# Performance work log

Measured on AMD Instinct MI355X. Metric: run time of the kernel, lower is better.

## Reference

```python
import jax, jax.numpy as jnp
import numpy as np

B, L, D, H = 64, 256, 512, 512


def setup_inputs() -> dict:
    key = jax.random.key(0)
    ks = jax.random.split(key, 17)
    s = 1.0 / np.sqrt(D + H)  # torch nn.Linear default init bound

    def w(k):
        return jax.random.uniform(k, (H, D + H), minval=-s, maxval=s, dtype=jnp.float32)

    def b(k):
        return jax.random.uniform(k, (H,), minval=-s, maxval=s, dtype=jnp.float32)

    inp = {"x": jax.random.normal(ks[0], (B, L, D), dtype=jnp.float32)}
    names = ["f", "i", "o", "g"]
    idx = 1
    for d in ("fw", "bw"):
        for n in names:
            kw, kb = jax.random.split(ks[idx])
            inp[f"W_{d}_{n}"] = w(kw)
            inp[f"b_{d}_{n}"] = b(kb)
            idx += 1
    return inp


def _make_cell(Wf, bf, Wi, bi, Wo, bo, Wg, bg):
    def cell(carry, xt):
        h, c = carry
        comb = jnp.concatenate([xt, h], axis=1)  # (B, D+H)
        ft = jax.nn.sigmoid(comb @ Wf.T + bf)
        it = jax.nn.sigmoid(comb @ Wi.T + bi)
        ot = jax.nn.sigmoid(comb @ Wo.T + bo)
        gt = jnp.tanh(comb @ Wg.T + bg)
        c = ft * c + it * gt
        h = ot * jnp.tanh(c)
        return (h, c), h
    return cell


def reference(x, W_fw_f, b_fw_f, W_fw_i, b_fw_i, W_fw_o, b_fw_o, W_fw_g, b_fw_g,
              W_bw_f, b_bw_f, W_bw_i, b_bw_i, W_bw_o, b_bw_o, W_bw_g, b_bw_g):
    Bx, Lx, _ = x.shape
    Hx = W_fw_f.shape[0]
    h0 = jnp.zeros((Bx, Hx), x.dtype)
    c0 = jnp.zeros((Bx, Hx), x.dtype)
    xs = jnp.swapaxes(x, 0, 1)  # (L, B, D) time-major

    _, hf = jax.lax.scan(_make_cell(W_fw_f, b_fw_f, W_fw_i, b_fw_i, W_fw_o, b_fw_o, W_fw_g, b_fw_g), (h0, c0), xs)
    _, hb = jax.lax.scan(_make_cell(W_bw_f, b_bw_f, W_bw_i, b_bw_i, W_bw_o, b_bw_o, W_bw_g, b_bw_g), (h0, c0), xs[::-1])
    hb = hb[::-1]  # hidden_b.reverse() in original

    # Faithful to original: stack time-major, flatten, hstack, reshape(B, L, 2H)
    flat = jnp.concatenate([hf.reshape(-1, Hx), hb.reshape(-1, Hx)], axis=1)  # (L*B, 2H)
    return flat.reshape(Bx, Lx, 2 * Hx)
```

## Files before the change

### kernel.cpp

```cpp
#include <hip/hip_runtime.h>

typedef unsigned short u16;
typedef unsigned int u32;
typedef unsigned long long u64;
typedef __bf16 bf16x8 __attribute__((ext_vector_type(8)));
typedef float f32x4 __attribute__((ext_vector_type(4)));

#define OFF_XPROJ 0ull
#define OFF_XBF   134217728ull
#define OFF_WXBF  150994944ull
#define OFF_BIAS  155189248ull
#define OFF_HRING 134217728ull
#define NSLOT 160
#define RESET_D 8

struct WPtrs { const float* p[8]; };

__device__ __forceinline__ u16 f2bf(float f) {
    __bf16 h = (__bf16)f;
    return __builtin_bit_cast(u16, h);
}
__device__ __forceinline__ float bf2f(u16 u) {
    __bf16 h = __builtin_bit_cast(__bf16, u);
    return (float)h;
}
__device__ __forceinline__ u32 pack2(float a, float b) {
    return (u32)f2bf(a) | ((u32)f2bf(b) << 16);
}
__device__ __forceinline__ float sigf(float x) {
    return __builtin_amdgcn_rcpf(1.0f + __expf(-x));
}
__device__ __forceinline__ float tanhfast(float x) {
    float a = fabsf(x);
    float e = __expf(-2.0f * a);
    float t = (1.0f - e) * __builtin_amdgcn_rcpf(1.0f + e);
    return copysignf(t, x);
}
__device__ __forceinline__ bool is_canary(u64 v) {
    return ((u32)v == 0xFFFFFFFFu) | ((u32)(v >> 32) == 0xFFFFFFFFu);
}

__global__ void __launch_bounds__(256) pack_x(const float* __restrict__ x, u16* __restrict__ xbf) {
    int idx = blockIdx.x * 256 + threadIdx.x;
    int e = idx * 4;
    float4 v = *(const float4*)(x + e);
    xbf[e+0] = f2bf(v.x); xbf[e+1] = f2bf(v.y);
    xbf[e+2] = f2bf(v.z); xbf[e+3] = f2bf(v.w);
}

__global__ void __launch_bounds__(256) pack_w(WPtrs wp, u16* __restrict__ wxbf) {
    int idx = blockIdx.x * 256 + threadIdx.x;
    int e = idx * 4;
    int n = e >> 9;
    int k = e & 511;
    int j = n & 511, g = (n >> 9) & 3, d = n >> 11;
    const float* W = wp.p[d*4 + g];
    float4 v = *(const float4*)(W + j*1024 + k);
    wxbf[n*512 + k + 0] = f2bf(v.x); wxbf[n*512 + k + 1] = f2bf(v.y);
    wxbf[n*512 + k + 2] = f2bf(v.z); wxbf[n*512 + k + 3] = f2bf(v.w);
}

__global__ void __launch_bounds__(256) pack_bias(WPtrs bp, u16* __restrict__ biasws) {
    int idx = blockIdx.x * 256 + threadIdx.x;
    int j = idx & 511, g = (idx >> 9) & 3, d = idx >> 11;
    biasws[idx] = f2bf(bp.p[d*4 + g][j]);
}

__global__ void __launch_bounds__(256) init_hring(u16* __restrict__ ring) {
    size_t idx = (size_t)blockIdx.x * 256 + threadIdx.x;
    size_t byte = idx * 16;
    size_t seg = byte % 10485760ull;
    uint4 v;
    if (seg < 65536ull) { v.x = 0u; v.y = 0u; v.z = 0u; v.w = 0u; }
    else                { v.x = ~0u; v.y = ~0u; v.z = ~0u; v.w = ~0u; }
    *(uint4*)((char*)ring + byte) = v;
}

__global__ void __launch_bounds__(256) gemm_xproj(const u16* __restrict__ xbf,
                                                  const u16* __restrict__ wxbf,
                                                  const u16* __restrict__ biasws,
                                                  u16* __restrict__ xproj) {
    __shared__ u16 A[64 * 264];
    int tid = threadIdx.x, w = tid >> 6, lane = tid & 63, q = lane >> 4, ln = lane & 15;
    int mb = blockIdx.x >> 6, nb = blockIdx.x & 63;
    int n = nb*64 + w*16 + ln;

    bf16x8 bfr[16];
    #pragma unroll
    for (int kk = 0; kk < 16; ++kk)
        bfr[kk] = *(const bf16x8*)(wxbf + n*512 + kk*32 + q*8);
    float bias = bf2f(biasws[n]);

    f32x4 acc[4] = {{0.f,0.f,0.f,0.f},{0.f,0.f,0.f,0.f},{0.f,0.f,0.f,0.f},{0.f,0.f,0.f,0.f}};
    const u16* Abase = xbf + (size_t)mb * 64 * 512;

    for (int half = 0; half < 2; ++half) {
        for (int it = 0; it < 8; ++it) {
            int idx = tid + it*256;
            int r = idx >> 5, c = idx & 31;
            *(uint4*)&A[r*264 + c*8] = *(const uint4*)(Abase + r*512 + half*256 + c*8);
        }
        __syncthreads();
        #pragma unroll
        for (int kk = 0; kk < 8; ++kk) {
            #pragma unroll
            for (int mt = 0; mt < 4; ++mt) {
                bf16x8 af = *(const bf16x8*)&A[(mt*16 + ln)*264 + kk*32 + q*8];
                acc[mt] = __builtin_amdgcn_mfma_f32_16x16x32_bf16(af, bfr[half*8 + kk], acc[mt], 0, 0, 0);
            }
        }
        __syncthreads();
    }

    int dd = n >> 11, gg = (n >> 9) & 3, jj = n & 511;
    #pragma unroll
    for (int mt = 0; mt < 4; ++mt) {
        #pragma unroll
        for (int r2 = 0; r2 < 4; ++r2) {
            int m = mb*64 + mt*16 + q*4 + r2;
            int t = m & 255, b = m >> 8;
            float v = acc[mt][r2] + bias;
            xproj[(size_t)((dd*256 + t)*64 + b) * 2048 + gg*512 + jj] = f2bf(v);
        }
    }
}

__global__ void __launch_bounds__(256) bilstm_rec(const u16* __restrict__ xproj,
                                                  u16* __restrict__ hring,
                                                  float* __restrict__ out,
                                                  WPtrs wp) {
    __shared__ u16 A[64 * 256];
    __shared__ float pre[4 * 64 * 17];

    int tid = threadIdx.x, w = tid >> 6, lane = tid & 63, q = lane >> 4, ln = lane & 15;
    int d = blockIdx.x >> 5, cb = blockIdx.x & 31, j0 = cb * 16;
    int b = tid >> 2, hc0 = (tid & 3) * 4;
    int col8h = tid & 63, rb = tid >> 7;
    bool phB = (tid & 64) != 0;

    const float* Wg = wp.p[d*4 + w];
    bf16x8 bfr[16];
    #pragma unroll
    for (int kk = 0; kk < 16; ++kk) {
        const float* src = Wg + (j0 + ln)*1024 + 512 + kk*32 + q*8;
        float4 v0 = *(const float4*)src;
        float4 v1 = *(const float4*)(src + 4);
        bf16x8 t;
        t[0]=(__bf16)v0.x; t[1]=(__bf16)v0.y; t[2]=(__bf16)v0.z; t[3]=(__bf16)v0.w;
        t[4]=(__bf16)v1.x; t[5]=(__bf16)v1.y; t[6]=(__bf16)v1.z; t[7]=(__bf16)v1.w;
        bfr[kk] = t;
    }

    float cre[4] = {0.f, 0.f, 0.f, 0.f};

    u64 xp4[4];
    {
        int t0 = d ? 255 : 0;
        const u16* xp_t = xproj + ((size_t)((d*256 + t0)*64 + b))*2048 + j0 + hc0;
        #pragma unroll
        for (int g = 0; g < 4; ++g) xp4[g] = *(const u64*)(xp_t + g*512);
    }

    for (int s = 0; s < 256; ++s) {
        int t_ = d ? (255 - s) : s;
        int sl = s;      if (sl >= NSLOT) sl -= NSLOT;
        int sw = s + 1;  if (sw >= NSLOT) sw -= NSLOT;
        int sr = s + 1 + RESET_D; if (sr >= NSLOT) sr -= NSLOT;
        const u64* hsrc = (const u64*)hring + ((size_t)(d*NSLOT + sl)) * 8192;

        u64 vv[32];
        {
            u64 v0 = __hip_atomic_load(hsrc + tid, __ATOMIC_RELAXED, __HIP_MEMORY_SCOPE_AGENT);
            while (is_canary(v0)) {
                __builtin_amdgcn_s_sleep(1);
                v0 = __hip_atomic_load(hsrc + tid, __ATOMIC_RELAXED, __HIP_MEMORY_SCOPE_AGENT);
            }
            vv[0] = v0;
        }
        #pragma unroll
        for (int it = 1; it < 32; ++it)
            vv[it] = __hip_atomic_load(hsrc + it*256 + tid, __ATOMIC_RELAXED, __HIP_MEMORY_SCOPE_AGENT);
        u32 pend = 0;
        #pragma unroll
        for (int it = 1; it < 32; ++it)
            if (is_canary(vv[it])) pend |= (1u << it);
        while (__builtin_expect(pend != 0u, 0)) {
            __builtin_amdgcn_s_sleep(1);
            u32 np = 0;
            #pragma unroll
            for (int it = 1; it < 32; ++it)
                if (pend & (1u << it)) {
                    u64 v = __hip_atomic_load(hsrc + it*256 + tid, __ATOMIC_RELAXED, __HIP_MEMORY_SCOPE_AGENT);
                    if (is_canary(v)) np |= (1u << it);
                    else vv[it] = v;
                }
            pend = np;
        }

        f32x4 acc[4] = {{0.f,0.f,0.f,0.f},{0.f,0.f,0.f,0.f},{0.f,0.f,0.f,0.f},{0.f,0.f,0.f,0.f}};

        if (!phB) {
            #pragma unroll
            for (int it = 0; it < 32; ++it) {
                int row = it*2 + rb;
                int off = row*512 + ((((col8h >> 1) ^ (row & 7)) << 4) | ((col8h & 1) << 3));
                *(u64*)((char*)A + off) = vv[it];
            }
        }
        __syncthreads();
        #pragma unroll
        for (int kk = 0; kk < 8; ++kk) {
            #pragma unroll
            for (int mt = 0; mt < 4; ++mt) {
                int row = mt*16 + ln;
                bf16x8 af = *(const bf16x8*)((const char*)A + row*512 + (((kk*4 + q) ^ (ln & 7)) << 4));
                acc[mt] = __builtin_amdgcn_mfma_f32_16x16x32_bf16(af, bfr[kk], acc[mt], 0, 0, 0);
            }
        }
        __syncthreads();

        if (phB) {
            #pragma unroll
            for (int it = 0; it < 32; ++it) {
                int row = it*2 + rb;
                int off = row*512 + ((((col8h >> 1) ^ (row & 7)) << 4) | ((col8h & 1) << 3));
                *(u64*)((char*)A + off) = vv[it];
            }
        }
        __syncthreads();
        #pragma unroll
        for (int kk = 0; kk < 8; ++kk) {
            #pragma unroll
            for (int mt = 0; mt < 4; ++mt) {
                int row = mt*16 + ln;
                bf16x8 af = *(const bf16x8*)((const char*)A + row*512 + (((kk*4 + q) ^ (ln & 7)) << 4));
                acc[mt] = __builtin_amdgcn_mfma_f32_16x16x32_bf16(af, bfr[8 + kk], acc[mt], 0, 0, 0);
            }
        }

        #pragma unroll
        for (int mt = 0; mt < 4; ++mt) {
            #pragma unroll
            for (int r2 = 0; r2 < 4; ++r2)
                pre[w*1088 + (mt*16 + q*4 + r2)*17 + ln] = acc[mt][r2];
        }
        __syncthreads();

        float h4[4];
        #pragma unroll
        for (int k = 0; k < 4; ++k) {
            int hc = hc0 + k;
            float fpre = pre[0*1088 + b*17 + hc] + bf2f((u16)(xp4[0] >> (16*k)));
            float ipre = pre[1*1088 + b*17 + hc] + bf2f((u16)(xp4[1] >> (16*k)));
            float opre = pre[2*1088 + b*17 + hc] + bf2f((u16)(xp4[2] >> (16*k)));
            float gpre = pre[3*1088 + b*17 + hc] + bf2f((u16)(xp4[3] >> (16*k)));
            float fg = sigf(fpre), ig = sigf(ipre), og = sigf(opre);
            float gg = tanhfast(gpre);
            float c = fg * cre[k] + ig * gg;
            cre[k] = c;
            h4[k] = og * tanhfast(c);
        }

        int wi = (b*512 + j0 + hc0) >> 2;
        {
            u64* hdst = (u64*)hring + ((size_t)(d*NSLOT + sw)) * 8192;
            u64 hv = (u64)pack2(h4[0], h4[1]) | ((u64)pack2(h4[2], h4[3]) << 32);
            __hip_atomic_store(hdst + wi, hv, __ATOMIC_RELAXED, __HIP_MEMORY_SCOPE_AGENT);
            u64* hrst = (u64*)hring + ((size_t)(d*NSLOT + sr)) * 8192;
            __hip_atomic_store(hrst + wi, ~0ull, __ATOMIC_RELAXED, __HIP_MEMORY_SCOPE_AGENT);
        }

        f32x4 o4 = { h4[0], h4[1], h4[2], h4[3] };
        __builtin_nontemporal_store(o4, (f32x4*)&out[(size_t)(t_*64 + b)*1024 + d*512 + j0 + hc0]);

        if (s + 1 < 256) {
            int tn = d ? (254 - s) : (s + 1);
            const u16* xp_t = xproj + ((size_t)((d*256 + tn)*64 + b))*2048 + j0 + hc0;
            #pragma unroll
            for (int g = 0; g < 4; ++g) xp4[g] = *(const u64*)(xp_t + g*512);
        }
    }
}

extern "C" void kernel_launch(void* const* d_in, const int* in_sizes, int n_in,
                              void* d_out, int out_size, void* d_ws, size_t ws_size,
                              hipStream_t stream) {
    const float* x = (const float*)d_in[0];
    WPtrs wp, bp;
    for (int d = 0; d < 2; ++d) {
        for (int g = 0; g < 4; ++g) {
            wp.p[d*4 + g] = (const float*)d_in[1 + d*8 + g*2];
            bp.p[d*4 + g] = (const float*)d_in[2 + d*8 + g*2];
        }
    }
    char* ws = (char*)d_ws;
    u16* xproj    = (u16*)(ws + OFF_XPROJ);
    u16* xbf      = (u16*)(ws + OFF_XBF);
    u16* wxbf     = (u16*)(ws + OFF_WXBF);
    u16* biasw    = (u16*)(ws + OFF_BIAS);
    u16* hring    = (u16*)(ws + OFF_HRING);
    float* out = (float*)d_out;

    hipLaunchKernelGGL(pack_x, dim3(8192), dim3(256), 0, stream, x, xbf);
    hipLaunchKernelGGL(pack_w, dim3(2048), dim3(256), 0, stream, wp, wxbf);
    hipLaunchKernelGGL(pack_bias, dim3(16), dim3(256), 0, stream, bp, biasw);
    hipLaunchKernelGGL(gemm_xproj, dim3(16384), dim3(256), 0, stream,
                       (const u16*)xbf, (const u16*)wxbf, (const u16*)biasw, xproj);
    hipLaunchKernelGGL(init_hring, dim3(5120), dim3(256), 0, stream, hring);

    const u16* xproj_c = xproj;
    void* args[] = { (void*)&xproj_c, (void*)&hring, (void*)&out, (void*)&wp };
    hipError_t err = hipLaunchCooperativeKernel((const void*)bilstm_rec, dim3(64), dim3(256), args, 0, stream);
    if (err != hipSuccess) {
        hipLaunchKernelGGL(bilstm_rec, dim3(64), dim3(256), 0, stream,
                           xproj_c, hring, out, wp);
    }
}
```

Baseline: 1.566 ms.

## Split recurrent step by batch per wave to remove block barriers and LDS gate exchange

Each wave now owns 16 batch rows and holds the weights for all four gates in registers, so the recurrent MFMAs compute f/i/o/g pre-activations for its rows directly. Each wave stages its own h rows in a private LDS region, which removes the __syncthreads barriers and the shared 'pre' buffer used to exchange gate results between waves. The xproj layout is interleaved by gate so each lane loads its four gate inputs with two 16-byte loads, and the canary-reset distance grows from 8 to 64 steps. This raises register pressure considerably (64 bf16x8 weight fragments per lane, launch_bounds 256,1), with a risk of spills.

```diff
diff --git a/kernel.cpp b/kernel.cpp
--- a/kernel.cpp
+++ b/kernel.cpp
@@ -12,7 +12,7 @@
 #define OFF_BIAS  155189248ull
 #define OFF_HRING 134217728ull
 #define NSLOT 160
-#define RESET_D 8
+#define RESET_D 64
 
 struct WPtrs { const float* p[8]; };
 
@@ -120,45 +120,46 @@
             int m = mb*64 + mt*16 + q*4 + r2;
             int t = m & 255, b = m >> 8;
             float v = acc[mt][r2] + bias;
-            xproj[(size_t)((dd*256 + t)*64 + b) * 2048 + gg*512 + jj] = f2bf(v);
-        }
-    }
-}
-
-__global__ void __launch_bounds__(256) bilstm_rec(const u16* __restrict__ xproj,
-                                                  u16* __restrict__ hring,
-                                                  float* __restrict__ out,
-                                                  WPtrs wp) {
-    __shared__ u16 A[64 * 256];
-    __shared__ float pre[4 * 64 * 17];
-
-    int tid = threadIdx.x, w = tid >> 6, lane = tid & 63, q = lane >> 4, ln = lane & 15;
+            xproj[(size_t)((dd*256 + t)*64 + b) * 2048 + jj*4 + gg] = f2bf(v);
+        }
+    }
+}
+
+__global__ void __launch_bounds__(256, 1) bilstm_rec(const u16* __restrict__ xproj,
+                                                     u16* __restrict__ hring,
+                                                     float* __restrict__ out,
+                                                     WPtrs wp) {
+    __shared__ u16 A[4 * 4096];
+
+    int tid = threadIdx.x, w = tid >> 6, l = tid & 63, q = l >> 4, ln = l & 15;
     int d = blockIdx.x >> 5, cb = blockIdx.x & 31, j0 = cb * 16;
-    int b = tid >> 2, hc0 = (tid & 3) * 4;
-    int col8h = tid & 63, rb = tid >> 7;
-    bool phB = (tid & 64) != 0;
-
-    const float* Wg = wp.p[d*4 + w];
-    bf16x8 bfr[16];
+    int b = w*16 + ln;
+    char* Aw = (char*)A + w * 8192;
+
+    bf16x8 bfr[4][16];
     #pragma unroll
-    for (int kk = 0; kk < 16; ++kk) {
-        const float* src = Wg + (j0 + ln)*1024 + 512 + kk*32 + q*8;
-        float4 v0 = *(const float4*)src;
-        float4 v1 = *(const float4*)(src + 4);
-        bf16x8 t;
-        t[0]=(__bf16)v0.x; t[1]=(__bf16)v0.y; t[2]=(__bf16)v0.z; t[3]=(__bf16)v0.w;
-        t[4]=(__bf16)v1.x; t[5]=(__bf16)v1.y; t[6]=(__bf16)v1.z; t[7]=(__bf16)v1.w;
-        bfr[kk] = t;
+    for (int g = 0; g < 4; ++g) {
+        const float* Wg = wp.p[d*4 + g];
+        #pragma unroll
+        for (int kk = 0; kk < 16; ++kk) {
+            const float* src = Wg + (j0 + ln)*1024 + 512 + kk*32 + q*8;
+            float4 v0 = *(const float4*)src;
+            float4 v1 = *(const float4*)(src + 4);
+            bf16x8 t;
+            t[0]=(__bf16)v0.x; t[1]=(__bf16)v0.y; t[2]=(__bf16)v0.z; t[3]=(__bf16)v0.w;
+            t[4]=(__bf16)v1.x; t[5]=(__bf16)v1.y; t[6]=(__bf16)v1.z; t[7]=(__bf16)v1.w;
+            bfr[g][kk] = t;
+        }
     }
 
     float cre[4] = {0.f, 0.f, 0.f, 0.f};
 
-    u64 xp4[4];
+    uint4 xpa, xpb;
     {
         int t0 = d ? 255 : 0;
-        const u16* xp_t = xproj + ((size_t)((d*256 + t0)*64 + b))*2048 + j0 + hc0;
-        #pragma unroll
-        for (int g = 0; g < 4; ++g) xp4[g] = *(const u64*)(xp_t + g*512);
+        const u16* p = xproj + ((size_t)((d*256 + t0)*64 + b))*2048 + (size_t)(j0 + q*4)*4;
+        xpa = *(const uint4*)p;
+        xpb = *(const uint4*)(p + 8);
     }
 
     for (int s = 0; s < 256; ++s) {
@@ -166,20 +167,21 @@
         int sl = s;      if (sl >= NSLOT) sl -= NSLOT;
         int sw = s + 1;  if (sw >= NSLOT) sw -= NSLOT;
         int sr = s + 1 + RESET_D; if (sr >= NSLOT) sr -= NSLOT;
-        const u64* hsrc = (const u64*)hring + ((size_t)(d*NSLOT + sl)) * 8192;
+        const u64* hsrc = (const u64*)hring + (size_t)(d*NSLOT + sl) * 8192;
 
         u64 vv[32];
         {
-            u64 v0 = __hip_atomic_load(hsrc + tid, __ATOMIC_RELAXED, __HIP_MEMORY_SCOPE_AGENT);
+            u64 v0 = __hip_atomic_load(hsrc + (size_t)(w*16)*128 + l, __ATOMIC_RELAXED, __HIP_MEMORY_SCOPE_AGENT);
             while (is_canary(v0)) {
                 __builtin_amdgcn_s_sleep(1);
-                v0 = __hip_atomic_load(hsrc + tid, __ATOMIC_RELAXED, __HIP_MEMORY_SCOPE_AGENT);
+                v0 = __hip_atomic_load(hsrc + (size_t)(w*16)*128 + l, __ATOMIC_RELAXED, __HIP_MEMORY_SCOPE_AGENT);
             }
             vv[0] = v0;
         }
         #pragma unroll
         for (int it = 1; it < 32; ++it)
-            vv[it] = __hip_atomic_load(hsrc + it*256 + tid, __ATOMIC_RELAXED, __HIP_MEMORY_SCOPE_AGENT);
+            vv[it] = __hip_atomic_load(hsrc + (size_t)(w*16 + (it >> 1))*128 + l + (it & 1)*64,
+                                       __ATOMIC_RELAXED, __HIP_MEMORY_SCOPE_AGENT);
         u32 pend = 0;
         #pragma unroll
         for (int it = 1; it < 32; ++it)
@@ -190,7 +192,8 @@
             #pragma unroll
             for (int it = 1; it < 32; ++it)
                 if (pend & (1u << it)) {
-                    u64 v = __hip_atomic_load(hsrc + it*256 + tid, __ATOMIC_RELAXED, __HIP_MEMORY_SCOPE_AGENT);
+                    u64 v = __hip_atomic_load(hsrc + (size_t)(w*16 + (it >> 1))*128 + l + (it & 1)*64,
+                                              __ATOMIC_RELAXED, __HIP_MEMORY_SCOPE_AGENT);
                     if (is_canary(v)) np |= (1u << it);
                     else vv[it] = v;
                 }
@@ -199,85 +202,76 @@
 
         f32x4 acc[4] = {{0.f,0.f,0.f,0.f},{0.f,0.f,0.f,0.f},{0.f,0.f,0.f,0.f},{0.f,0.f,0.f,0.f}};
 
-        if (!phB) {
-            #pragma unroll
-            for (int it = 0; it < 32; ++it) {
-                int row = it*2 + rb;
-                int off = row*512 + ((((col8h >> 1) ^ (row & 7)) << 4) | ((col8h & 1) << 3));
-                *(u64*)((char*)A + off) = vv[it];
+        #pragma unroll
+        for (int r = 0; r < 16; ++r) {
+            int off = r*512 + ((((l >> 1) ^ (r & 7)) << 4) | ((l & 1) << 3));
+            *(u64*)(Aw + off) = vv[r*2 + 0];
+        }
+        {
+            bf16x8 hf[8];
+            #pragma unroll
+            for (int kk = 0; kk < 8; ++kk)
+                hf[kk] = *(const bf16x8*)(Aw + ln*512 + (((kk*4 + q) ^ (ln & 7)) << 4));
+            #pragma unroll
+            for (int kk = 0; kk < 8; ++kk) {
+                #pragma unroll
+                for (int g = 0; g < 4; ++g)
+                    acc[g] = __builtin_amdgcn_mfma_f32_16x16x32_bf16(bfr[g][kk], hf[kk], acc[g], 0, 0, 0);
             }
         }
-        __syncthreads();
-        #pragma unroll
-        for (int kk = 0; kk < 8; ++kk) {
-            #pragma unroll
-            for (int mt = 0; mt < 4; ++mt) {
-                int row = mt*16 + ln;
-                bf16x8 af = *(const bf16x8*)((const char*)A + row*512 + (((kk*4 + q) ^ (ln & 7)) << 4));
-                acc[mt] = __builtin_amdgcn_mfma_f32_16x16x32_bf16(af, bfr[kk], acc[mt], 0, 0, 0);
+
+        #pragma unroll
+        for (int r = 0; r < 16; ++r) {
+            int off = r*512 + ((((l >> 1) ^ (r & 7)) << 4) | ((l & 1) << 3));
+            *(u64*)(Aw + off) = vv[r*2 + 1];
+        }
+        {
+            bf16x8 hf[8];
+            #pragma unroll
+            for (int kk = 0; kk < 8; ++kk)
+                hf[kk] = *(const bf16x8*)(Aw + ln*512 + (((kk*4 + q) ^ (ln & 7)) << 4));
+            #pragma unroll
+            for (int kk = 0; kk < 8; ++kk) {
+                #pragma unroll
+                for (int g = 0; g < 4; ++g)
+                    acc[g] = __builtin_amdgcn_mfma_f32_16x16x32_bf16(bfr[g][8 + kk], hf[kk], acc[g], 0, 0, 0);
             }
         }
-        __syncthreads();
-
-        if (phB) {
-            #pragma unroll
-            for (int it = 0; it < 32; ++it) {
-                int row = it*2 + rb;
-                int off = row*512 + ((((col8h >> 1) ^ (row & 7)) << 4) | ((col8h & 1) << 3));
-                *(u64*)((char*)A + off) = vv[it];
-            }
-        }
-        __syncthreads();
-        #pragma unroll
-        for (int kk = 0; kk < 8; ++kk) {
-            #pragma unroll
-            for (int mt = 0; mt < 4; ++mt) {
-                int row = mt*16 + ln;
-                bf16x8 af = *(const bf16x8*)((const char*)A + row*512 + (((kk*4 + q) ^ (ln & 7)) << 4));
-                acc[mt] = __builtin_amdgcn_mfma_f32_16x16x32_bf16(af, bfr[8 + kk], acc[mt], 0, 0, 0);
-            }
-        }
-
-        #pragma unroll
-        for (int mt = 0; mt < 4; ++mt) {
-            #pragma unroll
-            for (int r2 = 0; r2 < 4; ++r2)
-                pre[w*1088 + (mt*16 + q*4 + r2)*17 + ln] = acc[mt][r2];
-        }
-        __syncthreads();
-
+
+        u32 xq[8];
+        xq[0]=xpa.x; xq[1]=xpa.y; xq[2]=xpa.z; xq[3]=xpa.w;
+        xq[4]=xpb.x; xq[5]=xpb.y; xq[6]=xpb.z; xq[7]=xpb.w;
         float h4[4];
         #pragma unroll
-        for (int k = 0; k < 4; ++k) {
-            int hc = hc0 + k;
-            float fpre = pre[0*1088 + b*17 + hc] + bf2f((u16)(xp4[0] >> (16*k)));
-            float ipre = pre[1*1088 + b*17 + hc] + bf2f((u16)(xp4[1] >> (16*k)));
-            float opre = pre[2*1088 + b*17 + hc] + bf2f((u16)(xp4[2] >> (16*k)));
-            float gpre = pre[3*1088 + b*17 + hc] + bf2f((u16)(xp4[3] >> (16*k)));
+        for (int r2 = 0; r2 < 4; ++r2) {
+            float fpre = acc[0][r2] + bf2f((u16)(xq[r2*2]     & 0xFFFFu));
+            float ipre = acc[1][r2] + bf2f((u16)(xq[r2*2]     >> 16));
+            float opre = acc[2][r2] + bf2f((u16)(xq[r2*2 + 1] & 0xFFFFu));
+            float gpre = acc[3][r2] + bf2f((u16)(xq[r2*2 + 1] >> 16));
             float fg = sigf(fpre), ig = sigf(ipre), og = sigf(opre);
             float gg = tanhfast(gpre);
-            float c = fg * cre[k] + ig * gg;
-            cre[k] = c;
-            h4[k] = og * tanhfast(c);
-        }
-
-        int wi = (b*512 + j0 + hc0) >> 2;
+            float c = fg * cre[r2] + ig * gg;
+            cre[r2] = c;
+            h4[r2] = og * tanhfast(c);
+        }
+
         {
-            u64* hdst = (u64*)hring + ((size_t)(d*NSLOT + sw)) * 8192;
+            int wi = b*128 + cb*4 + q;
+            u64* hdst = (u64*)hring + (size_t)(d*NSLOT + sw) * 8192;
             u64 hv = (u64)pack2(h4[0], h4[1]) | ((u64)pack2(h4[2], h4[3]) << 32);
             __hip_atomic_store(hdst + wi, hv, __ATOMIC_RELAXED, __HIP_MEMORY_SCOPE_AGENT);
-            u64* hrst = (u64*)hring + ((size_t)(d*NSLOT + sr)) * 8192;
+            u64* hrst = (u64*)hring + (size_t)(d*NSLOT + sr) * 8192;
             __hip_atomic_store(hrst + wi, ~0ull, __ATOMIC_RELAXED, __HIP_MEMORY_SCOPE_AGENT);
         }
 
         f32x4 o4 = { h4[0], h4[1], h4[2], h4[3] };
-        __builtin_nontemporal_store(o4, (f32x4*)&out[(size_t)(t_*64 + b)*1024 + d*512 + j0 + hc0]);
+        __builtin_nontemporal_store(o4, (f32x4*)&out[(size_t)(t_*64 + b)*1024 + d*512 + j0 + q*4]);
 
         if (s + 1 < 256) {
             int tn = d ? (254 - s) : (s + 1);
-            const u16* xp_t = xproj + ((size_t)((d*256 + tn)*64 + b))*2048 + j0 + hc0;
-            #pragma unroll
-            for (int g = 0; g < 4; ++g) xp4[g] = *(const u64*)(xp_t + g*512);
+            const u16* p = xproj + ((size_t)((d*256 + tn)*64 + b))*2048 + (size_t)(j0 + q*4)*4;
+            xpa = *(const uint4*)p;
+            xpb = *(const uint4*)(p + 8);
         }
     }
 }
```

Result: faster. 1.520 ms (-3.0%).
